# Kernel tuning notes

Hardware: AMD Instinct MI355X
Metric: run time of the kernel (lower is better)

The kernel has to match this reference:

```python
import jax, jax.numpy as jnp
import numpy as np

EMBED_DIM = 1024
NUM_HEADS = 16
HEAD_DIM = EMBED_DIM // NUM_HEADS  # 64
KERNEL_SIZE = 64


def apply_rotary_emb(x, freqs_cos, freqs_sin):
    # x: [B, L, H, D]; freqs: [L, D//2]
    x_r = x[..., 0::2]
    x_i = x[..., 1::2]
    cos = freqs_cos[None, :, None, :]
    sin = freqs_sin[None, :, None, :]
    out_r = x_r * cos - x_i * sin
    out_i = x_r * sin + x_i * cos
    return jnp.stack([out_r, out_i], axis=-1).reshape(x.shape)


def setup_inputs() -> dict:
    key = jax.random.key(0)
    ks = jax.random.split(key, 8)
    B, L = 4, 4096
    x = jax.random.normal(ks[0], (B, L, EMBED_DIM), dtype=jnp.float32)
    freqs_cos = jax.random.normal(ks[1], (L, HEAD_DIM // 2), dtype=jnp.float32)
    freqs_sin = jax.random.normal(ks[2], (L, HEAD_DIM // 2), dtype=jnp.float32)
    attention_mask = jnp.ones((B, L), dtype=jnp.float32)
    scale = 1.0 / np.sqrt(EMBED_DIM)
    Wqkv = jax.random.normal(ks[3], (EMBED_DIM, 3 * EMBED_DIM), dtype=jnp.float32) * scale
    bqkv = jnp.zeros((3 * EMBED_DIM,), dtype=jnp.float32)
    proj = jax.random.normal(ks[4], (NUM_HEADS, HEAD_DIM, KERNEL_SIZE), dtype=jnp.float32) / np.sqrt(HEAD_DIM)
    Wout = jax.random.normal(ks[5], (EMBED_DIM, EMBED_DIM), dtype=jnp.float32) * scale
    bout = jnp.zeros((EMBED_DIM,), dtype=jnp.float32)
    return {"x": x, "freqs_cos": freqs_cos, "freqs_sin": freqs_sin,
            "attention_mask": attention_mask, "Wqkv": Wqkv, "bqkv": bqkv,
            "proj": proj, "Wout": Wout, "bout": bout}


def reference(x, freqs_cos, freqs_sin, attention_mask, Wqkv, bqkv, proj, Wout, bout):
    B, L, E = x.shape
    H, D = NUM_HEADS, HEAD_DIM
    qkv = x @ Wqkv + bqkv  # [B, L, 3E]
    q, k, v = jnp.split(qkv, 3, axis=-1)
    q = q.reshape(B, L, H, D)
    k = k.reshape(B, L, H, D)
    v = v.reshape(B, L, H, D)
    q = apply_rotary_emb(q, freqs_cos, freqs_sin)
    k = apply_rotary_emb(k, freqs_cos, freqs_sin)
    q = q.transpose(0, 2, 1, 3)  # [B, H, L, D]
    k = k.transpose(0, 2, 1, 3)
    v = v.transpose(0, 2, 1, 3)
    q_prime = jax.nn.relu(jnp.einsum('bhld,hdm->bhlm', q, proj))
    k_prime = jax.nn.relu(jnp.einsum('bhld,hdm->bhlm', k, proj))
    mask = attention_mask[:, None, :, None]  # [B, 1, L, 1]
    k_prime = k_prime * mask
    v = v * mask
    kv = jnp.einsum('bhlm,bhld->bhmd', k_prime, v)      # [B, H, M, D]
    context = jnp.einsum('bhlm,bhmd->bhld', q_prime, kv)  # [B, H, L, D]
    k_sum = k_prime.sum(axis=2)  # [B, H, M]
    norm = jnp.einsum('bhlm,bhm->bhl', q_prime, k_sum)
    output = context / (norm[..., None] + 0.0001)
    output = output.transpose(0, 2, 1, 3).reshape(B, L, E)
    return output @ Wout + bout
```

## Files before the change

kernel.cpp:

```cpp
#include <hip/hip_runtime.h>

#define LSEQ   4096
#define ROWS   16384
#define EMBED  1024
#define NHEADS 16
#define HDIM   64
#define QKV_N  3072

typedef __attribute__((ext_vector_type(8))) short bf16x8;
typedef __attribute__((ext_vector_type(8))) unsigned short u16x8;
typedef __attribute__((ext_vector_type(4))) float f32x4;

__device__ inline unsigned short bf16_rne(float x) {
    unsigned int u = __float_as_uint(x);
    unsigned int r = (u + 0x7fffu + ((u >> 16) & 1u)) >> 16;
    return (unsigned short)r;
}
__device__ inline float bf16_to_f32(unsigned short h) {
    return __uint_as_float(((unsigned int)h) << 16);
}

__device__ __forceinline__ int swz64(int row, int s) {
    return row * 64 + ((((s >> 3) ^ (row & 7))) << 3) + (s & 7);
}

__global__ __launch_bounds__(256)
void convert_hilo(const float* __restrict__ in, unsigned short* __restrict__ hi,
                  unsigned short* __restrict__ lo, int n)
{
    int i = (blockIdx.x * 256 + threadIdx.x) << 2;
    if (i >= n) return;
    float4 v = *reinterpret_cast<const float4*>(&in[i]);
    float a[4] = {v.x, v.y, v.z, v.w};
    unsigned short hh[4], ll[4];
    #pragma unroll
    for (int j = 0; j < 4; ++j) {
        hh[j] = bf16_rne(a[j]);
        ll[j] = bf16_rne(a[j] - bf16_to_f32(hh[j]));
    }
    *reinterpret_cast<ushort4*>(&hi[i]) = make_ushort4(hh[0], hh[1], hh[2], hh[3]);
    *reinterpret_cast<ushort4*>(&lo[i]) = make_ushort4(ll[0], ll[1], ll[2], ll[3]);
}

__global__ __launch_bounds__(256)
void convert_T_hilo(const float* __restrict__ in, unsigned short* __restrict__ hi,
                    unsigned short* __restrict__ lo, int K, int N)
{
    __shared__ float tile[64][65];
    const int n0 = blockIdx.x * 64, k0 = blockIdx.y * 64;
    const int t = threadIdx.x;
    #pragma unroll
    for (int i = 0; i < 16; ++i) {
        int idx = t + i * 256;
        int r = idx >> 6, c = idx & 63;
        tile[r][c] = in[(size_t)(k0 + r) * N + n0 + c];
    }
    __syncthreads();
    #pragma unroll
    for (int i = 0; i < 16; ++i) {
        int idx = t + i * 256;
        int r = idx >> 6, c = idx & 63;
        float v = tile[c][r];
        unsigned short h = bf16_rne(v);
        unsigned short l = bf16_rne(v - bf16_to_f32(h));
        size_t o = (size_t)(n0 + r) * K + k0 + c;
        hi[o] = h;
        lo[o] = l;
    }
}

__global__ __launch_bounds__(256)
void gemm3_kernel(const unsigned short* __restrict__ Ah, const unsigned short* __restrict__ Al,
                  const unsigned short* __restrict__ Bh, const unsigned short* __restrict__ Bl,
                  const float* __restrict__ bias, float* __restrict__ C,
                  int K, int ldc)
{
    __shared__ __align__(16) unsigned short lds[2][16384];

    const int t = threadIdx.x;
    const int wave = t >> 6, lane = t & 63;
    const int wr = wave >> 1, wc = wave & 1;
    const int rowBase = blockIdx.y * 128;
    const int colBase = blockIdx.x * 128;
    const int fr = lane & 15, fq = lane >> 4;

    const unsigned short* src = (wave == 0) ? Ah : (wave == 1) ? Al : (wave == 2) ? Bh : Bl;
    const int tileRow0 = (wave < 2) ? rowBase : colBase;
    const int ldsOff = wave * 4096;
    const int sRow = lane >> 2;
    const int sChunk = (((lane & 3) ^ ((lane >> 3) & 3)) << 3);

    f32x4 acc[4][4] = {};
    const int NT = K >> 5;

    #pragma unroll
    for (int i = 0; i < 8; ++i) {
        const unsigned short* g = src + (size_t)(tileRow0 + i * 16 + sRow) * K + sChunk;
        __builtin_amdgcn_global_load_lds(
            (const __attribute__((address_space(1))) void*)g,
            (__attribute__((address_space(3))) void*)&lds[0][ldsOff + i * 512], 16, 0, 0);
    }
    __syncthreads();

    for (int tI = 0; tI < NT; ++tI) {
        const int cur = tI & 1;

        if (tI + 1 < NT) {
            const int k0 = (tI + 1) << 5;
            #pragma unroll
            for (int i = 0; i < 8; ++i) {
                const unsigned short* g =
                    src + (size_t)(tileRow0 + i * 16 + sRow) * K + k0 + sChunk;
                __builtin_amdgcn_global_load_lds(
                    (const __attribute__((address_space(1))) void*)g,
                    (__attribute__((address_space(3))) void*)&lds[cur ^ 1][ldsOff + i * 512], 16, 0, 0);
            }
        }

        bf16x8 ah[4], al[4], bh[4], bl[4];
        #pragma unroll
        for (int m = 0; m < 4; ++m) {
            int r = wr * 64 + m * 16 + fr;
            int off = r * 32 + ((fq ^ ((r >> 1) & 3)) << 3);
            ah[m] = *reinterpret_cast<const bf16x8*>(&lds[cur][off]);
            al[m] = *reinterpret_cast<const bf16x8*>(&lds[cur][4096 + off]);
        }
        #pragma unroll
        for (int n = 0; n < 4; ++n) {
            int r = wc * 64 + n * 16 + fr;
            int off = r * 32 + ((fq ^ ((r >> 1) & 3)) << 3);
            bh[n] = *reinterpret_cast<const bf16x8*>(&lds[cur][8192 + off]);
            bl[n] = *reinterpret_cast<const bf16x8*>(&lds[cur][12288 + off]);
        }
        #pragma unroll
        for (int m = 0; m < 4; ++m)
            #pragma unroll
            for (int n = 0; n < 4; ++n) {
                acc[m][n] = __builtin_amdgcn_mfma_f32_16x16x32_bf16(ah[m], bh[n], acc[m][n], 0, 0, 0);
                acc[m][n] = __builtin_amdgcn_mfma_f32_16x16x32_bf16(ah[m], bl[n], acc[m][n], 0, 0, 0);
                acc[m][n] = __builtin_amdgcn_mfma_f32_16x16x32_bf16(al[m], bh[n], acc[m][n], 0, 0, 0);
            }

        __syncthreads();
    }

    #pragma unroll
    for (int m = 0; m < 4; ++m) {
        #pragma unroll
        for (int n = 0; n < 4; ++n) {
            int col = colBase + wc * 64 + n * 16 + fr;
            float bv = bias[col];
            #pragma unroll
            for (int r = 0; r < 4; ++r) {
                int row = rowBase + wr * 64 + m * 16 + fq * 4 + r;
                C[(size_t)row * ldc + col] = acc[m][n][r] + bv;
            }
        }
    }
}

__global__ __launch_bounds__(256)
void kv_mfma_kernel(const float* __restrict__ kvb, const float* __restrict__ cosb,
                    const float* __restrict__ sinb, const float* __restrict__ maskb,
                    const float* __restrict__ proj, float* __restrict__ partial)
{
    __shared__ __align__(16) char smem[66816];
    unsigned short* KR_h  = (unsigned short*)smem;
    unsigned short* KR_l  = (unsigned short*)(smem + 8192);
    float*          PS    = (float*)smem;
    unsigned short* PJT_h = (unsigned short*)(smem + 16384);
    unsigned short* PJT_l = (unsigned short*)(smem + 24576);
    unsigned short* KPT_h = (unsigned short*)(smem + 32768);
    unsigned short* KPT_l = (unsigned short*)(smem + 40960);
    unsigned short* VT_h  = (unsigned short*)(smem + 49152);
    unsigned short* VT_l  = (unsigned short*)(smem + 57344);
    float*          MS    = (float*)(smem + 65536);
    float*          KS    = (float*)(smem + 65792);

    const int chunk = blockIdx.x;
    const int hh    = blockIdx.y;
    const int t = threadIdx.x;
    const int w = t >> 6, lane = t & 63;
    const int fr = lane & 15, fq = lane >> 4;

    {
        int r = t >> 2, c0 = (t & 3) << 4;
        #pragma unroll
        for (int k = 0; k < 4; ++k)
            *reinterpret_cast<float4*>(&PS[r * 64 + c0 + k * 4]) =
                *reinterpret_cast<const float4*>(&proj[(size_t)hh * 4096 + r * 64 + c0 + k * 4]);
    }
    __syncthreads();
    {
        int m = t >> 2, d0 = (t & 3) << 4;
        unsigned short hb[16], lb[16];
        #pragma unroll
        for (int j = 0; j < 16; ++j) {
            float v = PS[(d0 + j) * 64 + m];
            hb[j] = bf16_rne(v);
            lb[j] = bf16_rne(v - bf16_to_f32(hb[j]));
        }
        #pragma unroll
        for (int cp = 0; cp < 2; ++cp) {
            u16x8 vh, vl;
            #pragma unroll
            for (int j = 0; j < 8; ++j) { vh[j] = hb[cp * 8 + j]; vl[j] = lb[cp * 8 + j]; }
            int sidx = swz64(m, d0 + cp * 8);
            *reinterpret_cast<u16x8*>(&PJT_h[sidx]) = vh;
            *reinterpret_cast<u16x8*>(&PJT_l[sidx]) = vl;
        }
    }
    __syncthreads();

    f32x4 acc2[4] = {};
    float ksacc[4] = {0.f, 0.f, 0.f, 0.f};

    for (int sub = 0; sub < 4; ++sub) {
        const int rowL = chunk * 256 + sub * 64;

        float4 vv[4];
        {
            int l = t >> 2, c0 = (t & 3) << 4;
            #pragma unroll
            for (int k2 = 0; k2 < 4; ++k2)
                vv[k2] = *reinterpret_cast<const float4*>(
                    &kvb[(size_t)(rowL + l) * 2048 + 1024 + hh * 64 + c0 + k2 * 4]);
        }
        #pragma unroll
        for (int i = 0; i < 8; ++i) {
            int p = t + (i << 8);
            int l = p >> 5, i2 = p & 31;
            size_t base = (size_t)(rowL + l) * 2048 + hh * 64 + 2 * i2;
            float kr = kvb[base], ki = kvb[base + 1];
            int crow = (rowL + l) & 4095;
            float c = cosb[(size_t)crow * 32 + i2];
            float s = sinb[(size_t)crow * 32 + i2];
            float xr = kr * c - ki * s;
            float xi = kr * s + ki * c;
            unsigned short h0 = bf16_rne(xr), h1 = bf16_rne(xi);
            unsigned short l0 = bf16_rne(xr - bf16_to_f32(h0));
            unsigned short l1 = bf16_rne(xi - bf16_to_f32(h1));
            int sidx = swz64(l, 2 * i2);
            *reinterpret_cast<unsigned int*>(&KR_h[sidx]) = (unsigned)h0 | ((unsigned)h1 << 16);
            *reinterpret_cast<unsigned int*>(&KR_l[sidx]) = (unsigned)l0 | ((unsigned)l1 << 16);
        }
        if (t < 64) MS[t] = maskb[rowL + t];
        __syncthreads();

        f32x4 acc1[4] = {};
        #pragma unroll
        for (int ks = 0; ks < 2; ++ks) {
            bf16x8 ah = *reinterpret_cast<const bf16x8*>(&KR_h[swz64(16 * w + fr, ks * 32 + fq * 8)]);
            bf16x8 al = *reinterpret_cast<const bf16x8*>(&KR_l[swz64(16 * w + fr, ks * 32 + fq * 8)]);
            #pragma unroll
            for (int n = 0; n < 4; ++n) {
                bf16x8 bh = *reinterpret_cast<const bf16x8*>(&PJT_h[swz64(16 * n + fr, ks * 32 + fq * 8)]);
                bf16x8 bl = *reinterpret_cast<const bf16x8*>(&PJT_l[swz64(16 * n + fr, ks * 32 + fq * 8)]);
                acc1[n] = __builtin_amdgcn_mfma_f32_16x16x32_bf16(ah, bh, acc1[n], 0, 0, 0);
                acc1[n] = __builtin_amdgcn_mfma_f32_16x16x32_bf16(ah, bl, acc1[n], 0, 0, 0);
                acc1[n] = __builtin_amdgcn_mfma_f32_16x16x32_bf16(al, bh, acc1[n], 0, 0, 0);
            }
        }
        #pragma unroll
        for (int n = 0; n < 4; ++n) {
            unsigned short hb[4], lb[4];
            float ssum = 0.f;
            #pragma unroll
            for (int r = 0; r < 4; ++r) {
                int l = 16 * w + fq * 4 + r;
                float kp = fmaxf(acc1[n][r], 0.f) * MS[l];
                ssum += kp;
                hb[r] = bf16_rne(kp);
                lb[r] = bf16_rne(kp - bf16_to_f32(hb[r]));
            }
            ksacc[n] += ssum;
            int sidx = swz64(16 * n + fr, 16 * w + fq * 4);
            *reinterpret_cast<ushort4*>(&KPT_h[sidx]) = make_ushort4(hb[0], hb[1], hb[2], hb[3]);
            *reinterpret_cast<ushort4*>(&KPT_l[sidx]) = make_ushort4(lb[0], lb[1], lb[2], lb[3]);
        }
        __syncthreads();

        {
            float* VS = PS;
            int l = t >> 2, c0 = (t & 3) << 4;
            float mv = MS[l];
            #pragma unroll
            for (int k2 = 0; k2 < 4; ++k2) {
                float4 q = vv[k2];
                q.x *= mv; q.y *= mv; q.z *= mv; q.w *= mv;
                *reinterpret_cast<float4*>(&VS[l * 64 + c0 + k2 * 4]) = q;
            }
        }
        __syncthreads();

        {
            float* VS = PS;
            int d = t >> 2, l0 = (t & 3) << 4;
            unsigned short hb[16], lb[16];
            #pragma unroll
            for (int j = 0; j < 16; ++j) {
                float v = VS[(l0 + j) * 64 + d];
                hb[j] = bf16_rne(v);
                lb[j] = bf16_rne(v - bf16_to_f32(hb[j]));
            }
            #pragma unroll
            for (int cp = 0; cp < 2; ++cp) {
                u16x8 vh, vl;
                #pragma unroll
                for (int j = 0; j < 8; ++j) { vh[j] = hb[cp * 8 + j]; vl[j] = lb[cp * 8 + j]; }
                int sidx = swz64(d, l0 + cp * 8);
                *reinterpret_cast<u16x8*>(&VT_h[sidx]) = vh;
                *reinterpret_cast<u16x8*>(&VT_l[sidx]) = vl;
            }
        }
        __syncthreads();

        #pragma unroll
        for (int ks = 0; ks < 2; ++ks) {
            bf16x8 ah = *reinterpret_cast<const bf16x8*>(&KPT_h[swz64(16 * w + fr, ks * 32 + fq * 8)]);
            bf16x8 al = *reinterpret_cast<const bf16x8*>(&KPT_l[swz64(16 * w + fr, ks * 32 + fq * 8)]);
            #pragma unroll
            for (int n = 0; n < 4; ++n) {
                bf16x8 bh = *reinterpret_cast<const bf16x8*>(&VT_h[swz64(16 * n + fr, ks * 32 + fq * 8)]);
                bf16x8 bl = *reinterpret_cast<const bf16x8*>(&VT_l[swz64(16 * n + fr, ks * 32 + fq * 8)]);
                acc2[n] = __builtin_amdgcn_mfma_f32_16x16x32_bf16(ah, bh, acc2[n], 0, 0, 0);
                acc2[n] = __builtin_amdgcn_mfma_f32_16x16x32_bf16(ah, bl, acc2[n], 0, 0, 0);
                acc2[n] = __builtin_amdgcn_mfma_f32_16x16x32_bf16(al, bh, acc2[n], 0, 0, 0);
            }
        }
    }

    #pragma unroll
    for (int n = 0; n < 4; ++n) {
        float v = ksacc[n];
        v += __shfl_xor(v, 16);
        v += __shfl_xor(v, 32);
        if (fq == 0) KS[w * 64 + 16 * n + fr] = v;
    }
    __syncthreads();

    float* dst = partial + ((size_t)hh * 64 + chunk) * 4160;
    #pragma unroll
    for (int n = 0; n < 4; ++n)
        #pragma unroll
        for (int r = 0; r < 4; ++r) {
            int m = 16 * w + fq * 4 + r;
            int d = 16 * n + fr;
            dst[m * 64 + d] = acc2[n][r];
        }
    if (t < 64)
        dst[4096 + t] = KS[t] + KS[64 + t] + KS[128 + t] + KS[192 + t];
}

__global__ __launch_bounds__(256)
void kv_reduce_kernel(const float* __restrict__ partial, float* __restrict__ kvout)
{
    const int bh = blockIdx.x;
    const int b = bh >> 4, h = bh & 15;
    const int seg = blockIdx.y;
    for (int idx = seg * 1040 + threadIdx.x; idx < (seg + 1) * 1040; idx += 256) {
        float s = 0.f;
        for (int c = 0; c < 16; ++c)
            s += partial[((size_t)h * 64 + b * 16 + c) * 4160 + idx];
        kvout[(size_t)bh * 4160 + idx] = s;
    }
}

__global__ __launch_bounds__(256)
void context_kernel(const float* __restrict__ qb, const float* __restrict__ cosb,
                    const float* __restrict__ sinb, const float* __restrict__ proj,
                    const float* __restrict__ kvsum, unsigned short* __restrict__ ch,
                    unsigned short* __restrict__ cl)
{
    const int lt = blockIdx.x;
    const int h  = blockIdx.y;
    const int t = threadIdx.x;
    const int bh = (lt >> 6) * 16 + h;

    __shared__ float bufA[64][68];
    __shared__ float qp[64][68];
    __shared__ float pj[64][64];
    __shared__ float ksum[64];

    for (int i = t; i < 1024; i += 256)
        *reinterpret_cast<float4*>(&pj[0][0] + (size_t)i * 4) =
            *reinterpret_cast<const float4*>(proj + (size_t)h * 4096 + (size_t)i * 4);
    if (t < 64) ksum[t] = kvsum[(size_t)bh * 4160 + 4096 + t];

    const int rowL = lt * 64;
    #pragma unroll
    for (int i = 0; i < 8; ++i) {
        int p = t + i * 256;
        int l = p >> 5, i2 = p & 31;
        size_t base = (size_t)(rowL + l) * 1024 + h * HDIM + 2 * i2;
        float qr = qb[base], qi = qb[base + 1];
        int crow = (rowL + l) & 4095;
        float c = cosb[(size_t)crow * 32 + i2];
        float s = sinb[(size_t)crow * 32 + i2];
        bufA[l][2 * i2]     = qr * c - qi * s;
        bufA[l][2 * i2 + 1] = qr * s + qi * c;
    }
    __syncthreads();

    {
        int l = t >> 2, m0 = (t & 3) << 4;
        float a[16] = {};
        for (int d = 0; d < 64; ++d) {
            float ql = bufA[l][d];
            const float* pr = &pj[d][m0];
            #pragma unroll
            for (int j = 0; j < 16; ++j) a[j] = fmaf(ql, pr[j], a[j]);
        }
        #pragma unroll
        for (int j = 0; j < 16; ++j) qp[l][m0 + j] = fmaxf(a[j], 0.f);
    }
    __syncthreads();

    #pragma unroll
    for (int i = 0; i < 4; ++i) {
        int idx = t + i * 256;
        int mm = idx >> 4, dd = (idx & 15) << 2;
        *reinterpret_cast<float4*>(&bufA[mm][dd]) =
            *reinterpret_cast<const float4*>(&kvsum[(size_t)bh * 4160 + mm * 64 + dd]);
    }
    __syncthreads();

    {
        int l = t >> 2, d0 = (t & 3) << 4;
        float a[16] = {};
        float nrm = 0.f;
        for (int mm = 0; mm < 64; ++mm) {
            float qv = qp[l][mm];
            nrm = fmaf(qv, ksum[mm], nrm);
            const float* kr = &bufA[mm][d0];
            #pragma unroll
            for (int j = 0; j < 16; ++j) a[j] = fmaf(qv, kr[j], a[j]);
        }
        float inv = 1.0f / (nrm + 1e-4f);
        size_t orow = (size_t)(rowL + l) * 1024 + h * HDIM + d0;
        #pragma unroll
        for (int j4 = 0; j4 < 4; ++j4) {
            unsigned short hh2[4], ll2[4];
            #pragma unroll
            for (int j = 0; j < 4; ++j) {
                float v = a[j4 * 4 + j] * inv;
                hh2[j] = bf16_rne(v);
                ll2[j] = bf16_rne(v - bf16_to_f32(hh2[j]));
            }
            *reinterpret_cast<ushort4*>(&ch[orow + j4 * 4]) = make_ushort4(hh2[0], hh2[1], hh2[2], hh2[3]);
            *reinterpret_cast<ushort4*>(&cl[orow + j4 * 4]) = make_ushort4(ll2[0], ll2[1], ll2[2], ll2[3]);
        }
    }
}

extern "C" void kernel_launch(void* const* d_in, const int* in_sizes, int n_in,
                              void* d_out, int out_size, void* d_ws, size_t ws_size,
                              hipStream_t stream)
{
    const float* x    = (const float*)d_in[0];
    const float* fcos = (const float*)d_in[1];
    const float* fsin = (const float*)d_in[2];
    const float* mask = (const float*)d_in[3];
    const float* Wqkv = (const float*)d_in[4];
    const float* bqkv = (const float*)d_in[5];
    const float* proj = (const float*)d_in[6];
    const float* Wout = (const float*)d_in[7];
    const float* bout = (const float*)d_in[8];
    float* out = (float*)d_out;

    float* W    = (float*)d_ws;
    float* XHL  = W + 4194304;
    float* KVQ  = XHL + 16777216;
    float* PART = KVQ + 33554432;
    float* KSUM = PART + 4259840;

    unsigned short* Wqh = (unsigned short*)W;
    unsigned short* Wql = Wqh + 3145728;
    unsigned short* Woh = Wql + 3145728;
    unsigned short* Wol = Woh + 1048576;
    unsigned short* xh  = (unsigned short*)XHL;
    unsigned short* xl  = xh + 16777216;

    convert_T_hilo<<<dim3(3072 / 64, 1024 / 64), 256, 0, stream>>>(Wqkv, Wqh, Wql, 1024, 3072);
    convert_T_hilo<<<dim3(1024 / 64, 1024 / 64), 256, 0, stream>>>(Wout, Woh, Wol, 1024, 1024);

    convert_hilo<<<16384, 256, 0, stream>>>(x, xh, xl, ROWS * EMBED);

    gemm3_kernel<<<dim3(2048 / 128, ROWS / 128), 256, 0, stream>>>(
        xh, xl, Wqh + (size_t)1024 * 1024, Wql + (size_t)1024 * 1024,
        bqkv + 1024, KVQ, 1024, 2048);

    kv_mfma_kernel<<<dim3(64, 16), 256, 0, stream>>>(KVQ, fcos, fsin, mask, proj, PART);

    kv_reduce_kernel<<<dim3(64, 4), 256, 0, stream>>>(PART, KSUM);

    gemm3_kernel<<<dim3(1024 / 128, ROWS / 128), 256, 0, stream>>>(
        xh, xl, Wqh, Wql, bqkv, KVQ, 1024, 1024);

    context_kernel<<<dim3(256, 16), 256, 0, stream>>>(
        KVQ, fcos, fsin, proj, KSUM, xh, xl);

    gemm3_kernel<<<dim3(1024 / 128, ROWS / 128), 256, 0, stream>>>(
        xh, xl, Woh, Wol, bout, out, 1024, 1024);
}
```

Before: 594.7 us.

## Enlarge split-bf16 GEMM tile to 256x256 with interleaved prefetch and barriers

The three-pass bf16 hi/lo GEMM now uses 512-thread blocks computing 256x256 output tiles, with each wave owning a 128x64 sub-tile (8x4 accumulators). The next K-slice's global-to-LDS loads are spread across four phases of the MFMA loop, with explicit s_barrier and waitcnt handling and raised wave priority during the MFMA bursts. The aim is more operand reuse per LDS byte, less global traffic, and better overlap of loads with matrix math. The cost is doubled LDS use (128KB), more accumulator registers, and fewer blocks per GEMM launch, which can lower occupancy and leave the grid too small to fill every CU.

```diff
diff --git a/kernel.cpp b/kernel.cpp
--- a/kernel.cpp
+++ b/kernel.cpp
@@ -69,28 +69,29 @@
     }
 }
 
-__global__ __launch_bounds__(256)
+__global__ __launch_bounds__(512)
 void gemm3_kernel(const unsigned short* __restrict__ Ah, const unsigned short* __restrict__ Al,
                   const unsigned short* __restrict__ Bh, const unsigned short* __restrict__ Bl,
                   const float* __restrict__ bias, float* __restrict__ C,
                   int K, int ldc)
 {
-    __shared__ __align__(16) unsigned short lds[2][16384];
+    __shared__ __align__(16) unsigned short lds[2][32768];
 
     const int t = threadIdx.x;
     const int wave = t >> 6, lane = t & 63;
-    const int wr = wave >> 1, wc = wave & 1;
-    const int rowBase = blockIdx.y * 128;
-    const int colBase = blockIdx.x * 128;
+    const int wr = wave >> 2, wc = wave & 3;
+    const int rowBase = blockIdx.y * 256;
+    const int colBase = blockIdx.x * 256;
     const int fr = lane & 15, fq = lane >> 4;
 
-    const unsigned short* src = (wave == 0) ? Ah : (wave == 1) ? Al : (wave == 2) ? Bh : Bl;
-    const int tileRow0 = (wave < 2) ? rowBase : colBase;
-    const int ldsOff = wave * 4096;
+    const int op = wave >> 1;
+    const unsigned short* src = (op == 0) ? Ah : (op == 1) ? Al : (op == 2) ? Bh : Bl;
+    const int tileRow0 = ((wave < 4) ? rowBase : colBase) + (wave & 1) * 128;
+    const int subOff = op * 8192 + (wave & 1) * 4096;
     const int sRow = lane >> 2;
     const int sChunk = (((lane & 3) ^ ((lane >> 3) & 3)) << 3);
 
-    f32x4 acc[4][4] = {};
+    f32x4 acc[8][4] = {};
     const int NT = K >> 5;
 
     #pragma unroll
@@ -98,61 +99,81 @@
         const unsigned short* g = src + (size_t)(tileRow0 + i * 16 + sRow) * K + sChunk;
         __builtin_amdgcn_global_load_lds(
             (const __attribute__((address_space(1))) void*)g,
-            (__attribute__((address_space(3))) void*)&lds[0][ldsOff + i * 512], 16, 0, 0);
+            (__attribute__((address_space(3))) void*)&lds[0][subOff + i * 512], 16, 0, 0);
     }
     __syncthreads();
 
     for (int tI = 0; tI < NT; ++tI) {
         const int cur = tI & 1;
-
-        if (tI + 1 < NT) {
-            const int k0 = (tI + 1) << 5;
-            #pragma unroll
-            for (int i = 0; i < 8; ++i) {
-                const unsigned short* g =
-                    src + (size_t)(tileRow0 + i * 16 + sRow) * K + k0 + sChunk;
-                __builtin_amdgcn_global_load_lds(
-                    (const __attribute__((address_space(1))) void*)g,
-                    (__attribute__((address_space(3))) void*)&lds[cur ^ 1][ldsOff + i * 512], 16, 0, 0);
-            }
-        }
-
-        bf16x8 ah[4], al[4], bh[4], bl[4];
-        #pragma unroll
-        for (int m = 0; m < 4; ++m) {
-            int r = wr * 64 + m * 16 + fr;
-            int off = r * 32 + ((fq ^ ((r >> 1) & 3)) << 3);
-            ah[m] = *reinterpret_cast<const bf16x8*>(&lds[cur][off]);
-            al[m] = *reinterpret_cast<const bf16x8*>(&lds[cur][4096 + off]);
-        }
-        #pragma unroll
-        for (int n = 0; n < 4; ++n) {
-            int r = wc * 64 + n * 16 + fr;
-            int off = r * 32 + ((fq ^ ((r >> 1) & 3)) << 3);
-            bh[n] = *reinterpret_cast<const bf16x8*>(&lds[cur][8192 + off]);
-            bl[n] = *reinterpret_cast<const bf16x8*>(&lds[cur][12288 + off]);
-        }
-        #pragma unroll
-        for (int m = 0; m < 4; ++m)
-            #pragma unroll
-            for (int n = 0; n < 4; ++n) {
-                acc[m][n] = __builtin_amdgcn_mfma_f32_16x16x32_bf16(ah[m], bh[n], acc[m][n], 0, 0, 0);
-                acc[m][n] = __builtin_amdgcn_mfma_f32_16x16x32_bf16(ah[m], bl[n], acc[m][n], 0, 0, 0);
-                acc[m][n] = __builtin_amdgcn_mfma_f32_16x16x32_bf16(al[m], bh[n], acc[m][n], 0, 0, 0);
-            }
-
-        __syncthreads();
-    }
-
-    #pragma unroll
-    for (int m = 0; m < 4; ++m) {
+        const unsigned short* ldsC = lds[cur];
+        const int k0 = (tI + 1) << 5;
+        const bool pref = (tI + 1 < NT);
+
+        bf16x8 bhf[4], blf[4];
+
+        #pragma unroll
+        for (int p = 0; p < 4; ++p) {
+            if (pref) {
+                const int i0 = (p == 0) ? 0 : (p == 1) ? 3 : (p == 2) ? 6 : 8;
+                const int i1 = (p == 0) ? 3 : (p == 1) ? 6 : (p == 2) ? 8 : 8;
+                for (int i = i0; i < i1; ++i) {
+                    const unsigned short* g =
+                        src + (size_t)(tileRow0 + i * 16 + sRow) * K + k0 + sChunk;
+                    __builtin_amdgcn_global_load_lds(
+                        (const __attribute__((address_space(1))) void*)g,
+                        (__attribute__((address_space(3))) void*)&lds[cur ^ 1][subOff + i * 512], 16, 0, 0);
+                }
+            }
+
+            bf16x8 ahf[2], alf[2];
+            #pragma unroll
+            for (int mm = 0; mm < 2; ++mm) {
+                int m = p * 2 + mm;
+                int r = wr * 128 + m * 16 + fr;
+                int off = r * 32 + ((fq ^ ((r >> 1) & 3)) << 3);
+                ahf[mm] = *reinterpret_cast<const bf16x8*>(&ldsC[off]);
+                alf[mm] = *reinterpret_cast<const bf16x8*>(&ldsC[8192 + off]);
+            }
+            if (p == 0) {
+                #pragma unroll
+                for (int n = 0; n < 4; ++n) {
+                    int rb = wc * 64 + n * 16 + fr;
+                    int off = rb * 32 + ((fq ^ ((rb >> 1) & 3)) << 3);
+                    bhf[n] = *reinterpret_cast<const bf16x8*>(&ldsC[16384 + off]);
+                    blf[n] = *reinterpret_cast<const bf16x8*>(&ldsC[24576 + off]);
+                }
+            }
+
+            __builtin_amdgcn_s_barrier();
+            asm volatile("s_waitcnt lgkmcnt(0)" ::: "memory");
+            __builtin_amdgcn_sched_barrier(0);
+            __builtin_amdgcn_s_setprio(1);
+            #pragma unroll
+            for (int mm = 0; mm < 2; ++mm) {
+                int m = p * 2 + mm;
+                #pragma unroll
+                for (int n = 0; n < 4; ++n) {
+                    acc[m][n] = __builtin_amdgcn_mfma_f32_16x16x32_bf16(ahf[mm], bhf[n], acc[m][n], 0, 0, 0);
+                    acc[m][n] = __builtin_amdgcn_mfma_f32_16x16x32_bf16(ahf[mm], blf[n], acc[m][n], 0, 0, 0);
+                    acc[m][n] = __builtin_amdgcn_mfma_f32_16x16x32_bf16(alf[mm], bhf[n], acc[m][n], 0, 0, 0);
+                }
+            }
+            __builtin_amdgcn_s_setprio(0);
+            if (p == 3)
+                asm volatile("s_waitcnt vmcnt(0)" ::: "memory");
+            __builtin_amdgcn_s_barrier();
+        }
+    }
+
+    #pragma unroll
+    for (int m = 0; m < 8; ++m) {
         #pragma unroll
         for (int n = 0; n < 4; ++n) {
             int col = colBase + wc * 64 + n * 16 + fr;
             float bv = bias[col];
             #pragma unroll
             for (int r = 0; r < 4; ++r) {
-                int row = rowBase + wr * 64 + m * 16 + fq * 4 + r;
+                int row = rowBase + wr * 128 + m * 16 + fq * 4 + r;
                 C[(size_t)row * ldc + col] = acc[m][n][r] + bv;
             }
         }
@@ -486,7 +507,7 @@
 
     convert_hilo<<<16384, 256, 0, stream>>>(x, xh, xl, ROWS * EMBED);
 
-    gemm3_kernel<<<dim3(2048 / 128, ROWS / 128), 256, 0, stream>>>(
+    gemm3_kernel<<<dim3(2048 / 256, ROWS / 256), 512, 0, stream>>>(
         xh, xl, Wqh + (size_t)1024 * 1024, Wql + (size_t)1024 * 1024,
         bqkv + 1024, KVQ, 1024, 2048);
 
@@ -494,12 +515,12 @@
 
     kv_reduce_kernel<<<dim3(64, 4), 256, 0, stream>>>(PART, KSUM);
 
-    gemm3_kernel<<<dim3(1024 / 128, ROWS / 128), 256, 0, stream>>>(
+    gemm3_kernel<<<dim3(1024 / 256, ROWS / 256), 512, 0, stream>>>(
         xh, xl, Wqh, Wql, bqkv, KVQ, 1024, 1024);
 
     context_kernel<<<dim3(256, 16), 256, 0, stream>>>(
         KVQ, fcos, fsin, proj, KSUM, xh, xl);
 
-    gemm3_kernel<<<dim3(1024 / 128, ROWS / 128), 256, 0, stream>>>(
+    gemm3_kernel<<<dim3(1024 / 256, ROWS / 256), 512, 0, stream>>>(
         xh, xl, Woh, Wol, bout, out, 1024, 1024);
 }
```

After: 517.3 us. -13.0%, faster.
